# Performance work log

Hardware: AMD Instinct MI355X
Metric: run time of the kernel (lower is better)

The kernel has to match this reference:

```python
import jax, jax.numpy as jnp
import numpy as np

B, S, H, NH = 2, 2048, 1024, 16
HD = H // NH  # head dim = 64


def setup_inputs() -> dict:
    key = jax.random.key(0)
    ks = jax.random.split(key, 11)
    s = 1.0 / np.sqrt(H)
    return {
        "q": jax.random.normal(ks[0], (B, S, H), jnp.float32),
        "k": jax.random.normal(ks[1], (B, S, H), jnp.float32),
        "v": jax.random.normal(ks[2], (B, S, H), jnp.float32),
        "Wq": jax.random.normal(ks[3], (H, H), jnp.float32) * s,
        "bq": jax.random.normal(ks[4], (H,), jnp.float32) * 0.02,
        "Wk": jax.random.normal(ks[5], (H, H), jnp.float32) * s,
        "bk": jax.random.normal(ks[6], (H,), jnp.float32) * 0.02,
        "Wv": jax.random.normal(ks[7], (H, H), jnp.float32) * s,
        "bv": jax.random.normal(ks[8], (H,), jnp.float32) * 0.02,
        "Wo": jax.random.normal(ks[9], (H, H), jnp.float32) * s,
        "bo": jax.random.normal(ks[10], (H,), jnp.float32) * 0.02,
    }


def reference(q, k, v, Wq, bq, Wk, bk, Wv, bv, Wo, bo):
    # QKV projections: [B,S,H]
    qp = q @ Wq + bq
    kp = k @ Wk + bk
    vp = v @ Wv + bv
    # split heads -> [B, NH, S, HD]
    def split(x):
        return x.reshape(B, S, NH, HD).transpose(0, 2, 1, 3)
    qh, kh, vh = split(qp), split(kp), split(vp)
    # scores [B, NH, S, S], scale by sqrt(head_dim)
    scores = jnp.einsum('bhqd,bhkd->bhqk', qh, kh) / jnp.sqrt(jnp.asarray(HD, qh.dtype))
    attn = jax.nn.softmax(scores, axis=-1)  # attention_dropout p=0.0 (eval)
    ctx = jnp.einsum('bhqk,bhkd->bhqd', attn, vh)
    # merge heads -> [B, S, H]
    ctx = ctx.transpose(0, 2, 1, 3).reshape(B, S, H)
    out = ctx @ Wo + bo  # dropout p=0.0 (eval)
    return out
```

## Files before the change

### kernel.cpp

```cpp
#include <hip/hip_runtime.h>

typedef unsigned short u16;
typedef __attribute__((ext_vector_type(8))) short bf16x8;
typedef __attribute__((ext_vector_type(4))) float f32x4;
typedef __attribute__((ext_vector_type(16))) float f32x16;
typedef __attribute__((ext_vector_type(4))) unsigned short u16x4;
typedef __attribute__((ext_vector_type(4))) unsigned int u32x4;

#define B_  2
#define S_  2048
#define H_  1024
#define NH_ 16
#define HD_ 64
#define MR_ (B_*S_)
#define K_  H_

__device__ __forceinline__ u16 f2bf(float f) {
  union { float f; unsigned u; } x; x.f = f;
  unsigned r = x.u + 0x7fffu + ((x.u >> 16) & 1u);
  return (u16)(r >> 16);
}

__device__ __forceinline__ unsigned cvtpk(float lo, float hi) {
  unsigned r;
  asm("v_cvt_pk_bf16_f32 %0, %1, %2" : "=v"(r) : "v"(lo), "v"(hi));
  return r;
}

__device__ __forceinline__ void plswap(unsigned &a, unsigned &b) {
  asm("v_permlane32_swap_b32 %0, %1" : "+v"(a), "+v"(b));
}

__device__ __forceinline__ void gload16(const u16* g, u16* l) {
  __builtin_amdgcn_global_load_lds((const __attribute__((address_space(1))) void*)g,
                                   (__attribute__((address_space(3))) void*)l, 16, 0, 0);
}

__global__ __launch_bounds__(256) void cvt3(const float* __restrict__ q, const float* __restrict__ k,
                                            const float* __restrict__ v, u16* __restrict__ dst) {
  const float* src = blockIdx.z == 0 ? q : blockIdx.z == 1 ? k : v;
  u16* d = dst + (size_t)blockIdx.z * MR_ * H_;
  size_t i = ((size_t)blockIdx.x * 256 + threadIdx.x) * 4;
  float4 f = *(const float4*)(src + i);
  u16x4 o = { f2bf(f.x), f2bf(f.y), f2bf(f.z), f2bf(f.w) };
  *(u16x4*)(d + i) = o;
}

__global__ __launch_bounds__(256) void wtrans(const float* __restrict__ Wq, const float* __restrict__ Wk,
                                              const float* __restrict__ Wv, const float* __restrict__ Wo,
                                              u16* __restrict__ wt) {
  const int z = blockIdx.z;
  const float* W = z == 0 ? Wq : z == 1 ? Wk : z == 2 ? Wv : Wo;
  u16* Wt = wt + (size_t)z * H_ * K_;
  __shared__ float t[32][33];
  const int n0 = blockIdx.x * 32, k0 = blockIdx.y * 32;
  const int tx = threadIdx.x & 31, ty = threadIdx.x >> 5;
  #pragma unroll
  for (int i = 0; i < 4; i++) t[ty + 8*i][tx] = W[(size_t)(k0 + ty + 8*i) * H_ + n0 + tx];
  __syncthreads();
  #pragma unroll
  for (int i = 0; i < 4; i++) Wt[(size_t)(n0 + ty + 8*i) * K_ + k0 + tx] = f2bf(t[tx][ty + 8*i]);
}

template <int MODE>
__device__ __forceinline__ void gemm_body(const u16* __restrict__ A, const u16* __restrict__ Bt,
                                          const float* __restrict__ bias, float scale,
                                          u16* __restrict__ Obf, float* __restrict__ Of,
                                          int m_tile, int n_tile) {
  __shared__ u16 ldsA[128 * 64];
  __shared__ u16 ldsB[128 * 64];
  const int tid = threadIdx.x;
  const int lane = tid & 63, wave = tid >> 6;
  const int wm = wave >> 1, wn = wave & 1;
  const int m0 = m_tile * 128, n0 = n_tile * 128;

  f32x4 acc[4][4] = {};

  const int srow = tid >> 3;
  const int sslot = (tid & 7) ^ (srow & 7);
  const u16* ga = A + (size_t)(m0 + srow) * K_ + sslot * 8;
  const u16* gb = Bt + (size_t)(n0 + srow) * K_ + sslot * 8;
  u16* la = ldsA + tid * 8;
  u16* lb = ldsB + tid * 8;

  const int fr = lane & 15;
  const int kg = lane >> 4;

  for (int k0 = 0; k0 < K_; k0 += 64) {
    #pragma unroll
    for (int j = 0; j < 4; j++) gload16(ga + (size_t)(j * 32) * K_ + k0, la + j * 2048);
    #pragma unroll
    for (int j = 0; j < 4; j++) gload16(gb + (size_t)(j * 32) * K_ + k0, lb + j * 2048);
    __syncthreads();

    #pragma unroll
    for (int kk = 0; kk < 2; kk++) {
      const int ps = (((kk << 2) | kg) ^ (fr & 7)) * 8;
      bf16x8 a[4], b[4];
      #pragma unroll
      for (int mf = 0; mf < 4; mf++)
        a[mf] = *(const bf16x8*)&ldsA[(wm * 64 + mf * 16 + fr) * 64 + ps];
      #pragma unroll
      for (int nf = 0; nf < 4; nf++)
        b[nf] = *(const bf16x8*)&ldsB[(wn * 64 + nf * 16 + fr) * 64 + ps];
      #pragma unroll
      for (int mf = 0; mf < 4; mf++)
        #pragma unroll
        for (int nf = 0; nf < 4; nf++)
          acc[mf][nf] = __builtin_amdgcn_mfma_f32_16x16x32_bf16(a[mf], b[nf], acc[mf][nf], 0, 0, 0);
    }
    __syncthreads();
  }

  float bcol[4];
  #pragma unroll
  for (int nf = 0; nf < 4; nf++) bcol[nf] = bias[n0 + wn * 64 + nf * 16 + fr];

  if (MODE == 2) {
    #pragma unroll
    for (int mf = 0; mf < 4; mf++) {
      const int row0 = m0 + wm * 64 + mf * 16 + kg * 4;
      #pragma unroll
      for (int nf = 0; nf < 4; nf++) {
        const int col = n0 + wn * 64 + nf * 16 + fr;
        u16x4 o;
        #pragma unroll
        for (int r = 0; r < 4; r++) o[r] = f2bf(acc[mf][nf][r] + bcol[nf]);
        size_t idx = (((size_t)(col + ((row0 >> 11) << 10))) << 11) + (row0 & 2047);
        *(u16x4*)(Obf + idx) = o;
      }
    }
  } else {
    #pragma unroll
    for (int mf = 0; mf < 4; mf++)
      #pragma unroll
      for (int r = 0; r < 4; r++) {
        const int row = m0 + wm * 64 + mf * 16 + kg * 4 + r;
        #pragma unroll
        for (int nf = 0; nf < 4; nf++) {
          const int col = n0 + wn * 64 + nf * 16 + fr;
          float val = (acc[mf][nf][r] + bcol[nf]) * scale;
          if (MODE == 0) Obf[(size_t)row * H_ + col] = f2bf(val);
          else           Of [(size_t)row * H_ + col] = val;
        }
      }
  }
}

__device__ __forceinline__ void gemm_tiles(int &m_tile, int &n_tile) {
  const int bid = blockIdx.x + (blockIdx.y << 3);
  const int swz = ((bid & 7) << 5) + (bid >> 3);
  m_tile = swz >> 3;
  n_tile = swz & 7;
}

__global__ __launch_bounds__(256) void gemm_qkv(const u16* __restrict__ xb, const u16* __restrict__ wt,
                                                const float* __restrict__ b0, const float* __restrict__ b1,
                                                const float* __restrict__ b2,
                                                u16* __restrict__ QKo, u16* __restrict__ VTo) {
  const int z = blockIdx.z;
  const u16* A = xb + (size_t)z * MR_ * K_;
  const u16* Bt = wt + (size_t)z * H_ * K_;
  int mt, nt;
  gemm_tiles(mt, nt);
  if (z == 2) {
    gemm_body<2>(A, Bt, b2, 1.0f, VTo, nullptr, mt, nt);
  } else {
    const float* bias = z == 0 ? b0 : b1;
    const float scale = z == 0 ? 0.18033688011112042f : 1.0f;
    gemm_body<0>(A, Bt, bias, scale, QKo + (size_t)z * MR_ * H_, nullptr, mt, nt);
  }
}

__global__ __launch_bounds__(256) void gemm_out(const u16* __restrict__ ctx, const u16* __restrict__ wot,
                                                const float* __restrict__ bo, float* __restrict__ out) {
  int mt, nt;
  gemm_tiles(mt, nt);
  gemm_body<1>(ctx, wot, bo, 1.0f, nullptr, out, mt, nt);
}

__global__ __launch_bounds__(512) void attn(const u16* __restrict__ qp, const u16* __restrict__ kp,
                                            const u16* __restrict__ vt, u16* __restrict__ ctx) {
  __shared__ u16 Kl[2][2][64 * 64];
  __shared__ u16 Vl[2][2][64 * 64];
  __shared__ float mlbuf[2][4][32][2];
  const int bid = blockIdx.x + (blockIdx.y << 4);
  const int swz = ((bid & 7) << 6) + (bid >> 3);
  const int bh = swz >> 4;
  const int b = bh >> 4, h = bh & 15;
  const int q0 = (swz & 15) * 128;
  const int tid = threadIdx.x;
  const int g0 = tid >> 8;
  const int gt = tid & 255;
  const int w = (tid >> 6) & 3;
  const int l = tid & 63;
  const int ql = l & 31, hi = l >> 5;

  const u16* Q   = qp + (size_t)b * S_ * H_ + h * HD_;
  const u16* Kb  = kp + (size_t)b * S_ * H_ + h * HD_;
  const u16* Vtb = vt + (size_t)bh * HD_ * S_;
  u16* O = ctx + (size_t)b * S_ * H_ + h * HD_;

  const int srow = gt >> 3;
  const int sslot = (gt & 7) ^ (srow & 7);
  const int sbase = g0 << 10;

  const int qrow = q0 + w * 32 + ql;
  bf16x8 qf[4];
  #pragma unroll
  for (int ds = 0; ds < 4; ds++)
    qf[ds] = *(const bf16x8*)&Q[(size_t)qrow * H_ + ds * 16 + hi * 8];

  f32x16 oacc0 = {}, oacc1 = {};
  float m_run = -1e30f, l_run = 0.f;

  #pragma unroll
  for (int j = 0; j < 2; j++) {
    gload16(Kb + (size_t)(sbase + srow + 32 * j) * H_ + sslot * 8,
            &Kl[g0][0][0] + j * 2048 + gt * 8);
    gload16(Vtb + (size_t)(srow + 32 * j) * S_ + sbase + sslot * 8,
            &Vl[g0][0][0] + j * 2048 + gt * 8);
  }

  for (int it = 0; it < 16; ++it) {
    const int s0 = sbase + it * 64, cur = it & 1;
    __syncthreads();
    if (it + 1 < 16) {
      #pragma unroll
      for (int j = 0; j < 2; j++) {
        gload16(Kb + (size_t)(s0 + 64 + srow + 32 * j) * H_ + sslot * 8,
                &Kl[g0][cur ^ 1][0] + j * 2048 + gt * 8);
        gload16(Vtb + (size_t)(srow + 32 * j) * S_ + s0 + 64 + sslot * 8,
                &Vl[g0][cur ^ 1][0] + j * 2048 + gt * 8);
      }
    }
    f32x16 sc0 = {}, sc1 = {};
    __builtin_amdgcn_s_setprio(1);
    #pragma unroll
    for (int ds = 0; ds < 4; ds++) {
      const int sl = ((ds * 2 + hi) ^ (ql & 7)) << 3;
      bf16x8 k0 = *(const bf16x8*)&Kl[g0][cur][ql * 64 + sl];
      bf16x8 k1 = *(const bf16x8*)&Kl[g0][cur][(32 + ql) * 64 + sl];
      sc0 = __builtin_amdgcn_mfma_f32_32x32x16_bf16(k0, qf[ds], sc0, 0, 0, 0);
      sc1 = __builtin_amdgcn_mfma_f32_32x32x16_bf16(k1, qf[ds], sc1, 0, 0, 0);
    }
    __builtin_amdgcn_s_setprio(0);
    float t4[8];
    #pragma unroll
    for (int g = 0; g < 4; g++) {
      t4[g]     = fmaxf(fmaxf(sc0[4*g], sc0[4*g+1]), fmaxf(sc0[4*g+2], sc0[4*g+3]));
      t4[4 + g] = fmaxf(fmaxf(sc1[4*g], sc1[4*g+1]), fmaxf(sc1[4*g+2], sc1[4*g+3]));
    }
    float tmax = fmaxf(fmaxf(fmaxf(t4[0], t4[1]), fmaxf(t4[2], t4[3])),
                       fmaxf(fmaxf(t4[4], t4[5]), fmaxf(t4[6], t4[7])));
    tmax = fmaxf(tmax, __shfl_xor(tmax, 32, 64));
    if (!__all(tmax <= m_run + 8.0f)) {
      const float mn = fmaxf(m_run, tmax);
      const float sf = __builtin_amdgcn_exp2f(m_run - mn);
      m_run = mn;
      l_run *= sf;
      #pragma unroll
      for (int r = 0; r < 16; r++) {
        const float sfq = __shfl(sf, (r & 3) + 8 * (r >> 2) + 4 * hi, 64);
        oacc0[r] *= sfq;
        oacc1[r] *= sfq;
      }
    }
    float ps4[8];
    #pragma unroll
    for (int g = 0; g < 4; g++) {
      #pragma unroll
      for (int m = 0; m < 4; m++) {
        sc0[4*g+m] = __builtin_amdgcn_exp2f(sc0[4*g+m] - m_run);
        sc1[4*g+m] = __builtin_amdgcn_exp2f(sc1[4*g+m] - m_run);
      }
      ps4[g]     = (sc0[4*g] + sc0[4*g+1]) + (sc0[4*g+2] + sc0[4*g+3]);
      ps4[4 + g] = (sc1[4*g] + sc1[4*g+1]) + (sc1[4*g+2] + sc1[4*g+3]);
    }
    float psum = ((ps4[0] + ps4[1]) + (ps4[2] + ps4[3])) + ((ps4[4] + ps4[5]) + (ps4[6] + ps4[7]));
    psum += __shfl_xor(psum, 32, 64);
    l_run += psum;
    uint2 pk0[4], pk1[4];
    #pragma unroll
    for (int g = 0; g < 4; g++) {
      pk0[g].x = cvtpk(sc0[4*g], sc0[4*g+1]);  pk0[g].y = cvtpk(sc0[4*g+2], sc0[4*g+3]);
      pk1[g].x = cvtpk(sc1[4*g], sc1[4*g+1]);  pk1[g].y = cvtpk(sc1[4*g+2], sc1[4*g+3]);
    }
    __builtin_amdgcn_s_setprio(1);
    #pragma unroll
    for (int ks = 0; ks < 4; ks++) {
      const int ga = (ks & 1) * 2;
      unsigned x0, y0, x1, y1;
      if (ks < 2) { x0 = pk0[ga].x; y0 = pk0[ga].y; x1 = pk0[ga+1].x; y1 = pk0[ga+1].y; }
      else        { x0 = pk1[ga].x; y0 = pk1[ga].y; x1 = pk1[ga+1].x; y1 = pk1[ga+1].y; }
      plswap(x0, x1);
      plswap(y0, y1);
      u32x4 fu = { x0, y0, x1, y1 };
      const bf16x8 pfrag = __builtin_bit_cast(bf16x8, fu);
      #pragma unroll
      for (int dt = 0; dt < 2; dt++) {
        const int d = dt * 32 + ql;
        bf16x8 vf = *(const bf16x8*)&Vl[g0][cur][d * 64 + (((ks * 2 + hi) ^ (d & 7)) << 3)];
        if (dt == 0) oacc0 = __builtin_amdgcn_mfma_f32_32x32x16_bf16(pfrag, vf, oacc0, 0, 0, 0);
        else         oacc1 = __builtin_amdgcn_mfma_f32_32x32x16_bf16(pfrag, vf, oacc1, 0, 0, 0);
      }
    }
    __builtin_amdgcn_s_setprio(0);
  }

  if (l < 32) { mlbuf[g0][w][ql][0] = m_run; mlbuf[g0][w][ql][1] = l_run; }
  __syncthreads();
  const float m_o = mlbuf[g0 ^ 1][w][ql][0];
  const float l_o = mlbuf[g0 ^ 1][w][ql][1];
  const float m_tot = fmaxf(m_run, m_o);
  const float a_s = __builtin_amdgcn_exp2f(m_run - m_tot);
  const float rinv = 1.0f / (l_run * a_s + l_o * __builtin_amdgcn_exp2f(m_o - m_tot));
  float ar[16], rr[16];
  #pragma unroll
  for (int r = 0; r < 16; r++) {
    const int qi = (r & 3) + 8 * (r >> 2) + 4 * hi;
    ar[r] = __shfl(a_s, qi, 64);
    rr[r] = __shfl(rinv, qi, 64);
  }

  float* cb = (float*)(&Kl[0][0][0]);
  float* cw = cb + w * 2048 + l;
  if (g0 == 1) {
    #pragma unroll
    for (int r = 0; r < 16; r++) {
      cw[r * 64]        = oacc0[r] * ar[r];
      cw[(16 + r) * 64] = oacc1[r] * ar[r];
    }
  }
  __syncthreads();
  if (g0 == 0) {
    #pragma unroll
    for (int r = 0; r < 16; r++) {
      const int qi = (r & 3) + 8 * (r >> 2) + 4 * hi;
      const int row = q0 + w * 32 + qi;
      O[(size_t)row * H_ + ql]      = f2bf((oacc0[r] * ar[r] + cw[r * 64]) * rr[r]);
      O[(size_t)row * H_ + 32 + ql] = f2bf((oacc1[r] * ar[r] + cw[(16 + r) * 64]) * rr[r]);
    }
  }
}

extern "C" void kernel_launch(void* const* d_in, const int* in_sizes, int n_in,
                              void* d_out, int out_size, void* d_ws, size_t ws_size,
                              hipStream_t stream) {
  const float* q  = (const float*)d_in[0];
  const float* k  = (const float*)d_in[1];
  const float* v  = (const float*)d_in[2];
  const float* Wq = (const float*)d_in[3];
  const float* bq = (const float*)d_in[4];
  const float* Wk = (const float*)d_in[5];
  const float* bk = (const float*)d_in[6];
  const float* Wv = (const float*)d_in[7];
  const float* bv = (const float*)d_in[8];
  const float* Wo = (const float*)d_in[9];
  const float* bo = (const float*)d_in[10];
  float* out = (float*)d_out;

  char* ws = (char*)d_ws;
  const size_t MB = 1024 * 1024;
  u16* xb   = (u16*)(ws);
  u16* wt   = (u16*)(ws + 24 * MB);
  u16* qkp  = (u16*)(ws + 32 * MB);
  u16* vtp  = (u16*)(ws + 48 * MB);
  u16* ctx  = (u16*)(ws);

  cvt3  <<<dim3(4096, 1, 3), 256, 0, stream>>>(q, k, v, xb);
  wtrans<<<dim3(32, 32, 4),  256, 0, stream>>>(Wq, Wk, Wv, Wo, wt);
  gemm_qkv<<<dim3(8, 32, 3), 256, 0, stream>>>(xb, wt, bq, bk, bv, qkp, vtp);
  attn  <<<dim3(16, 32),     512, 0, stream>>>(qkp, qkp + (size_t)MR_ * H_, vtp, ctx);
  gemm_out<<<dim3(8, 32, 1), 256, 0, stream>>>(ctx, wt + (size_t)3 * H_ * K_, bo, out);
}
```

Baseline: 143.0 us.

## Merge prep kernels, reload Q fragments per tile, raise attn occupancy bound

Fuses the input bf16 conversion and weight transpose kernels into one launch to save a kernel launch and tail. In attention, Q fragments are no longer held in registers across the loop but reloaded from global memory each iteration, and launch bounds now request 4 blocks of 512 threads per CU, which caps VGPR use. The register cap is meant to raise occupancy, at the cost of repeated global Q loads and possible spilling.

```diff
diff --git a/kernel.cpp b/kernel.cpp
--- a/kernel.cpp
+++ b/kernel.cpp
@@ -36,30 +36,34 @@
                                    (__attribute__((address_space(3))) void*)l, 16, 0, 0);
 }
 
-__global__ __launch_bounds__(256) void cvt3(const float* __restrict__ q, const float* __restrict__ k,
-                                            const float* __restrict__ v, u16* __restrict__ dst) {
-  const float* src = blockIdx.z == 0 ? q : blockIdx.z == 1 ? k : v;
-  u16* d = dst + (size_t)blockIdx.z * MR_ * H_;
-  size_t i = ((size_t)blockIdx.x * 256 + threadIdx.x) * 4;
-  float4 f = *(const float4*)(src + i);
-  u16x4 o = { f2bf(f.x), f2bf(f.y), f2bf(f.z), f2bf(f.w) };
-  *(u16x4*)(d + i) = o;
-}
-
-__global__ __launch_bounds__(256) void wtrans(const float* __restrict__ Wq, const float* __restrict__ Wk,
-                                              const float* __restrict__ Wv, const float* __restrict__ Wo,
-                                              u16* __restrict__ wt) {
-  const int z = blockIdx.z;
-  const float* W = z == 0 ? Wq : z == 1 ? Wk : z == 2 ? Wv : Wo;
-  u16* Wt = wt + (size_t)z * H_ * K_;
+__global__ __launch_bounds__(256) void prep(const float* __restrict__ q, const float* __restrict__ k,
+                                            const float* __restrict__ v, const float* __restrict__ Wq,
+                                            const float* __restrict__ Wk, const float* __restrict__ Wv,
+                                            const float* __restrict__ Wo, u16* __restrict__ dst,
+                                            u16* __restrict__ wt) {
   __shared__ float t[32][33];
-  const int n0 = blockIdx.x * 32, k0 = blockIdx.y * 32;
-  const int tx = threadIdx.x & 31, ty = threadIdx.x >> 5;
-  #pragma unroll
-  for (int i = 0; i < 4; i++) t[ty + 8*i][tx] = W[(size_t)(k0 + ty + 8*i) * H_ + n0 + tx];
-  __syncthreads();
-  #pragma unroll
-  for (int i = 0; i < 4; i++) Wt[(size_t)(n0 + ty + 8*i) * K_ + k0 + tx] = f2bf(t[tx][ty + 8*i]);
+  const int bid = blockIdx.x;
+  if (bid < 12288) {
+    const int z = bid >> 12;
+    const float* src = z == 0 ? q : z == 1 ? k : v;
+    u16* d = dst + (size_t)z * MR_ * H_;
+    size_t i = ((size_t)(bid & 4095) * 256 + threadIdx.x) * 4;
+    float4 f = *(const float4*)(src + i);
+    u16x4 o = { f2bf(f.x), f2bf(f.y), f2bf(f.z), f2bf(f.w) };
+    *(u16x4*)(d + i) = o;
+  } else {
+    const int r = bid - 12288;
+    const int z = r >> 10;
+    const float* W = z == 0 ? Wq : z == 1 ? Wk : z == 2 ? Wv : Wo;
+    u16* Wt = wt + (size_t)z * H_ * K_;
+    const int n0 = (r & 31) * 32, k0 = ((r >> 5) & 31) * 32;
+    const int tx = threadIdx.x & 31, ty = threadIdx.x >> 5;
+    #pragma unroll
+    for (int i = 0; i < 4; i++) t[ty + 8*i][tx] = W[(size_t)(k0 + ty + 8*i) * H_ + n0 + tx];
+    __syncthreads();
+    #pragma unroll
+    for (int i = 0; i < 4; i++) Wt[(size_t)(n0 + ty + 8*i) * K_ + k0 + tx] = f2bf(t[tx][ty + 8*i]);
+  }
 }
 
 template <int MODE>
@@ -179,8 +183,8 @@
   gemm_body<1>(ctx, wot, bo, 1.0f, nullptr, out, mt, nt);
 }
 
-__global__ __launch_bounds__(512) void attn(const u16* __restrict__ qp, const u16* __restrict__ kp,
-                                            const u16* __restrict__ vt, u16* __restrict__ ctx) {
+__global__ __launch_bounds__(512, 4) void attn(const u16* __restrict__ qp, const u16* __restrict__ kp,
+                                               const u16* __restrict__ vt, u16* __restrict__ ctx) {
   __shared__ u16 Kl[2][2][64 * 64];
   __shared__ u16 Vl[2][2][64 * 64];
   __shared__ float mlbuf[2][4][32][2];
@@ -205,11 +209,7 @@
   const int sslot = (gt & 7) ^ (srow & 7);
   const int sbase = g0 << 10;
 
-  const int qrow = q0 + w * 32 + ql;
-  bf16x8 qf[4];
-  #pragma unroll
-  for (int ds = 0; ds < 4; ds++)
-    qf[ds] = *(const bf16x8*)&Q[(size_t)qrow * H_ + ds * 16 + hi * 8];
+  const u16* Qrow = Q + (size_t)(q0 + w * 32 + ql) * H_;
 
   f32x16 oacc0 = {}, oacc1 = {};
   float m_run = -1e30f, l_run = 0.f;
@@ -239,10 +239,11 @@
     #pragma unroll
     for (int ds = 0; ds < 4; ds++) {
       const int sl = ((ds * 2 + hi) ^ (ql & 7)) << 3;
+      bf16x8 qd = *(const bf16x8*)&Qrow[ds * 16 + hi * 8];
       bf16x8 k0 = *(const bf16x8*)&Kl[g0][cur][ql * 64 + sl];
       bf16x8 k1 = *(const bf16x8*)&Kl[g0][cur][(32 + ql) * 64 + sl];
-      sc0 = __builtin_amdgcn_mfma_f32_32x32x16_bf16(k0, qf[ds], sc0, 0, 0, 0);
-      sc1 = __builtin_amdgcn_mfma_f32_32x32x16_bf16(k1, qf[ds], sc1, 0, 0, 0);
+      sc0 = __builtin_amdgcn_mfma_f32_32x32x16_bf16(k0, qd, sc0, 0, 0, 0);
+      sc1 = __builtin_amdgcn_mfma_f32_32x32x16_bf16(k1, qd, sc1, 0, 0, 0);
     }
     __builtin_amdgcn_s_setprio(0);
     float t4[8];
@@ -368,8 +369,7 @@
   u16* vtp  = (u16*)(ws + 48 * MB);
   u16* ctx  = (u16*)(ws);
 
-  cvt3  <<<dim3(4096, 1, 3), 256, 0, stream>>>(q, k, v, xb);
-  wtrans<<<dim3(32, 32, 4),  256, 0, stream>>>(Wq, Wk, Wv, Wo, wt);
+  prep  <<<dim3(16384),      256, 0, stream>>>(q, k, v, Wq, Wk, Wv, Wo, xb, wt);
   gemm_qkv<<<dim3(8, 32, 3), 256, 0, stream>>>(xb, wt, bq, bk, bv, qkp, vtp);
   attn  <<<dim3(16, 32),     512, 0, stream>>>(qkp, qkp + (size_t)MR_ * H_, vtp, ctx);
   gemm_out<<<dim3(8, 32, 1), 256, 0, stream>>>(ctx, wt + (size_t)3 * H_ * K_, bo, out);
```

Result: faster. 132.9 us (-7.1%).
